# Kernel optimization log

Hardware: AMD Instinct MI355X
Metric: run time of the kernel (lower is better)

## Reference

```python
import jax, jax.numpy as jnp
import numpy as np

N_NODES = 100000
N_EDGES = 1600000
IN_C, HID_C, OUT_C = 128, 128, 64
N_LAYERS, K, ALPHA = 4, 10, 0.1
LN_EPS = 1e-5


def setup_inputs() -> dict:
    key = jax.random.key(0)
    k1, k2, k3, k4, k5 = jax.random.split(key, 5)
    x = jax.random.normal(k1, (N_NODES, IN_C), dtype=jnp.float32)
    edge_index = jax.random.randint(k2, (2, N_EDGES), 0, N_NODES, dtype=jnp.int64)
    edge_weight = jax.random.uniform(k3, (N_EDGES,), dtype=jnp.float32)
    # Learned parameters (torch Linear default init scale ~ 1/sqrt(fan_in))
    W_enc = jax.random.normal(k4, (HID_C, IN_C), dtype=jnp.float32) / np.sqrt(IN_C)
    W_dec = jax.random.normal(k5, (OUT_C, HID_C), dtype=jnp.float32) / np.sqrt(HID_C)
    gamma = jnp.ones((HID_C,), dtype=jnp.float32)
    beta = jnp.zeros((HID_C,), dtype=jnp.float32)
    return {"x": x, "edge_index": edge_index, "edge_weight": edge_weight,
            "W_enc": W_enc, "W_dec": W_dec, "gamma": gamma, "beta": beta}


def _layer_norm(z, gamma, beta):
    mu = jnp.mean(z, axis=-1, keepdims=True)
    var = jnp.mean(jnp.square(z - mu), axis=-1, keepdims=True)
    return gamma * (z - mu) * jax.lax.rsqrt(var + LN_EPS) + beta


def _appnp(h, src, dst, w):
    # K-step personalized-pagerank propagation; normalize=False -> raw edge_weight
    x0 = h
    def step(_, z):
        msg = z[src] * w[:, None]                       # [E, HID_C] gather + scale
        agg = jax.ops.segment_sum(msg, dst, num_segments=N_NODES)  # scatter-add
        return (1.0 - ALPHA) * agg + ALPHA * x0
    return jax.lax.fori_loop(0, K, step, h)


def reference(x, edge_index, edge_weight, W_enc, W_dec, gamma, beta):
    src, dst = edge_index[0], edge_index[1]  # message flows source -> target
    h = x @ W_enc.T
    h = jax.nn.gelu(_layer_norm(h, gamma, beta), approximate=False)
    for _ in range(N_LAYERS):
        h = jax.nn.gelu(_appnp(h, src, dst, edge_weight), approximate=False)
        h = _layer_norm(h, gamma, beta)
    out = h @ W_dec.T
    return jnp.squeeze(out)
```

## Files before the change

### kernel.cpp

```cpp
#include <hip/hip_runtime.h>
#include <math.h>

#define N_NODES 100000
#define N_EDGES 1600000
#define IN_C 128
#define HID_C 128
#define OUT_C 64
#define NLAYERS 4
#define KSTEPS 10
#define ALPHA 0.1f
#define LN_EPS 1e-5f

#define SCAN_N (N_NODES + 1)
#define SCAN_BLOCKS ((SCAN_N + 1023) / 1024)
#define EP_CAP 2400000

__device__ __forceinline__ float gelu_exact(float x) {
    return 0.5f * x * (1.0f + erff(x * 0.70710678118654752f));
}

__device__ __forceinline__ unsigned pack_bf16_rne(float a, float b) {
    unsigned ua = __float_as_uint(a);
    unsigned ub = __float_as_uint(b);
    ua = (ua + 0x7fffu + ((ua >> 16) & 1u)) >> 16;
    ub = (ub + 0x7fffu + ((ub >> 16) & 1u)) >> 16;
    return (ub << 16) | ua;
}
__device__ __forceinline__ float bf_lo(unsigned d) { return __uint_as_float(d << 16); }
__device__ __forceinline__ float bf_hi(unsigned d) { return __uint_as_float(d & 0xffff0000u); }

__global__ void count_k(const int* __restrict__ dst, int* __restrict__ counts) {
    int e = blockIdx.x * blockDim.x + threadIdx.x;
    if (e < N_EDGES) atomicAdd(&counts[dst[e]], 1);
}

__global__ __launch_bounds__(1024) void scan1_k(const int* __restrict__ counts,
                                                int* __restrict__ bsum) {
    __shared__ int s[1024];
    int i = blockIdx.x * 1024 + threadIdx.x;
    int c = 0;
    if (i < N_NODES) c = (counts[i] + 7) & ~7;
    s[threadIdx.x] = c;
    __syncthreads();
    for (int off = 512; off; off >>= 1) {
        if (threadIdx.x < off) s[threadIdx.x] += s[threadIdx.x + off];
        __syncthreads();
    }
    if (threadIdx.x == 0) bsum[blockIdx.x] = s[0];
}

__global__ void scan2_k(int* __restrict__ bsum) {
    __shared__ int s[128];
    int t = threadIdx.x;
    s[t] = (t < SCAN_BLOCKS) ? bsum[t] : 0;
    __syncthreads();
    for (int off = 1; off < 128; off <<= 1) {
        int v = (t >= off) ? s[t - off] : 0;
        __syncthreads();
        s[t] += v;
        __syncthreads();
    }
    if (t < SCAN_BLOCKS) bsum[t] = (t == 0) ? 0 : s[t - 1];
}

__global__ __launch_bounds__(1024) void scan3_k(const int* __restrict__ counts,
                                                const int* __restrict__ bsum,
                                                int* __restrict__ row_off,
                                                int* __restrict__ fill_pos) {
    __shared__ int s[1024];
    int i = blockIdx.x * 1024 + threadIdx.x;
    int c = 0;
    if (i < N_NODES) c = (counts[i] + 7) & ~7;
    s[threadIdx.x] = c;
    __syncthreads();
    for (int off = 1; off < 1024; off <<= 1) {
        int v = (threadIdx.x >= off) ? s[threadIdx.x - off] : 0;
        __syncthreads();
        s[threadIdx.x] += v;
        __syncthreads();
    }
    if (i <= N_NODES) {
        int excl = s[threadIdx.x] - c + bsum[blockIdx.x];
        row_off[i] = excl;
        fill_pos[i] = excl;
    }
}

__global__ void bucket_k(const int* __restrict__ src, const int* __restrict__ dst,
                         const float* __restrict__ w,
                         int* __restrict__ fill_pos, int2* __restrict__ ep) {
    int e = blockIdx.x * blockDim.x + threadIdx.x;
    if (e >= N_EDGES) return;
    int d = dst[e];
    int pos = atomicAdd(&fill_pos[d], 1);
    float ws = (1.0f - ALPHA) * w[e];
    ep[pos] = make_int2(src[e] << 6, __float_as_int(ws));
}

__global__ __launch_bounds__(1024) void encoder_k(
        const float* __restrict__ x, const float* __restrict__ Wenc,
        const float* __restrict__ gamma, const float* __restrict__ beta,
        unsigned* __restrict__ H) {
    __shared__ float WT[IN_C * 130];
    __shared__ float XS[16][512];
    for (int i = threadIdx.x; i < IN_C * HID_C; i += 1024) {
        int c = i >> 7, k = i & 127;
        WT[k * 130 + c] = Wenc[i];
    }
    __syncthreads();
    int lane = threadIdx.x & 63;
    int wid  = threadIdx.x >> 6;
    const float2* WT2 = (const float2*)WT;
    float2 gb = ((const float2*)gamma)[lane];
    float2 bb = ((const float2*)beta)[lane];
    int wstride = gridDim.x * 16;
    float* xs = XS[wid];
    for (int grp = blockIdx.x * 16 + wid; grp * 4 < N_NODES; grp += wstride) {
        int r0 = grp * 4;
        const float4* xr = (const float4*)(x + (size_t)r0 * IN_C);
        ((float4*)xs)[lane]      = xr[lane];
        ((float4*)xs)[64 + lane] = xr[64 + lane];
        __builtin_amdgcn_wave_barrier();
        float a0x = 0, a0y = 0, a1x = 0, a1y = 0;
        float a2x = 0, a2y = 0, a3x = 0, a3y = 0;
        const float4* xs4 = (const float4*)xs;
#pragma unroll 4
        for (int k4 = 0; k4 < 32; ++k4) {
            float4 xv0 = xs4[k4];
            float4 xv1 = xs4[32 + k4];
            float4 xv2 = xs4[64 + k4];
            float4 xv3 = xs4[96 + k4];
            int k = k4 * 4;
            float2 w0 = WT2[(k + 0) * 65 + lane];
            float2 w1 = WT2[(k + 1) * 65 + lane];
            float2 w2 = WT2[(k + 2) * 65 + lane];
            float2 w3 = WT2[(k + 3) * 65 + lane];
#define ENC_ROW(ax, ay, xv)                                      \
            ax = fmaf(xv.x, w0.x, ax); ay = fmaf(xv.x, w0.y, ay); \
            ax = fmaf(xv.y, w1.x, ax); ay = fmaf(xv.y, w1.y, ay); \
            ax = fmaf(xv.z, w2.x, ax); ay = fmaf(xv.z, w2.y, ay); \
            ax = fmaf(xv.w, w3.x, ax); ay = fmaf(xv.w, w3.y, ay);
            ENC_ROW(a0x, a0y, xv0)
            ENC_ROW(a1x, a1y, xv1)
            ENC_ROW(a2x, a2y, xv2)
            ENC_ROW(a3x, a3y, xv3)
#undef ENC_ROW
        }
        __builtin_amdgcn_wave_barrier();
#define ENC_EPI(ax, ay, row)                                               \
        {                                                                   \
            float sum = ax + ay;                                            \
            for (int off = 32; off; off >>= 1) sum += __shfl_xor(sum, off); \
            float mu = sum * (1.0f / 128.0f);                               \
            float d0 = ax - mu, d1 = ay - mu;                               \
            float vs = d0 * d0 + d1 * d1;                                   \
            for (int off = 32; off; off >>= 1) vs += __shfl_xor(vs, off);   \
            float inv = rsqrtf(vs * (1.0f / 128.0f) + LN_EPS);              \
            float o0 = gelu_exact(gb.x * d0 * inv + bb.x);                  \
            float o1 = gelu_exact(gb.y * d1 * inv + bb.y);                  \
            H[(size_t)(row)*64 + lane] = pack_bf16_rne(o0, o1);             \
        }
        ENC_EPI(a0x, a0y, r0)
        ENC_EPI(a1x, a1y, r0 + 1)
        ENC_EPI(a2x, a2y, r0 + 2)
        ENC_EPI(a3x, a3y, r0 + 3)
#undef ENC_EPI
    }
}

__global__ __launch_bounds__(256) void prop_k(
        const unsigned* __restrict__ zin, const unsigned* __restrict__ x0,
        const int* __restrict__ row_off, const int2* __restrict__ ep,
        unsigned* __restrict__ zout, int fuse_ln,
        const float* __restrict__ gamma, const float* __restrict__ beta) {
    int gw = (blockIdx.x * 256 + threadIdx.x) >> 6;
    if (gw >= N_NODES) return;
    int lane = threadIdx.x & 63;
    int s0 = row_off[gw];
    int s1 = row_off[gw + 1];
    float sx = 0.f, sy = 0.f;
    for (int base = s0; base < s1; base += 64) {
        int cnt = min(64, s1 - base);
        int2 p = make_int2(0, 0);
        if (lane < cnt) p = ep[base + lane];
        for (int j = 0; j < cnt; j += 8) {
            int   o0 = __shfl(p.x, j + 0); float w0 = __int_as_float(__shfl(p.y, j + 0));
            int   o1 = __shfl(p.x, j + 1); float w1 = __int_as_float(__shfl(p.y, j + 1));
            int   o2 = __shfl(p.x, j + 2); float w2 = __int_as_float(__shfl(p.y, j + 2));
            int   o3 = __shfl(p.x, j + 3); float w3 = __int_as_float(__shfl(p.y, j + 3));
            int   o4 = __shfl(p.x, j + 4); float w4 = __int_as_float(__shfl(p.y, j + 4));
            int   o5 = __shfl(p.x, j + 5); float w5 = __int_as_float(__shfl(p.y, j + 5));
            int   o6 = __shfl(p.x, j + 6); float w6 = __int_as_float(__shfl(p.y, j + 6));
            int   o7 = __shfl(p.x, j + 7); float w7 = __int_as_float(__shfl(p.y, j + 7));
            unsigned d0 = zin[o0 + lane];
            unsigned d1 = zin[o1 + lane];
            unsigned d2 = zin[o2 + lane];
            unsigned d3 = zin[o3 + lane];
            unsigned d4 = zin[o4 + lane];
            unsigned d5 = zin[o5 + lane];
            unsigned d6 = zin[o6 + lane];
            unsigned d7 = zin[o7 + lane];
            sx = fmaf(w0, bf_lo(d0), sx); sy = fmaf(w0, bf_hi(d0), sy);
            sx = fmaf(w1, bf_lo(d1), sx); sy = fmaf(w1, bf_hi(d1), sy);
            sx = fmaf(w2, bf_lo(d2), sx); sy = fmaf(w2, bf_hi(d2), sy);
            sx = fmaf(w3, bf_lo(d3), sx); sy = fmaf(w3, bf_hi(d3), sy);
            sx = fmaf(w4, bf_lo(d4), sx); sy = fmaf(w4, bf_hi(d4), sy);
            sx = fmaf(w5, bf_lo(d5), sx); sy = fmaf(w5, bf_hi(d5), sy);
            sx = fmaf(w6, bf_lo(d6), sx); sy = fmaf(w6, bf_hi(d6), sy);
            sx = fmaf(w7, bf_lo(d7), sx); sy = fmaf(w7, bf_hi(d7), sy);
        }
    }
    unsigned xd = x0[(size_t)gw * 64 + lane];
    float zx = fmaf(ALPHA, bf_lo(xd), sx);
    float zy = fmaf(ALPHA, bf_hi(xd), sy);
    unsigned od;
    if (fuse_ln) {
        float h0 = gelu_exact(zx);
        float h1 = gelu_exact(zy);
        float sum = h0 + h1;
        for (int off = 32; off; off >>= 1) sum += __shfl_xor(sum, off);
        float mu = sum * (1.0f / 128.0f);
        float d0 = h0 - mu, d1 = h1 - mu;
        float vs = d0 * d0 + d1 * d1;
        for (int off = 32; off; off >>= 1) vs += __shfl_xor(vs, off);
        float inv = rsqrtf(vs * (1.0f / 128.0f) + LN_EPS);
        float2 gb = ((const float2*)gamma)[lane];
        float2 bb = ((const float2*)beta)[lane];
        od = pack_bf16_rne(gb.x * d0 * inv + bb.x, gb.y * d1 * inv + bb.y);
    } else {
        od = pack_bf16_rne(zx, zy);
    }
    zout[(size_t)gw * 64 + lane] = od;
}

__global__ __launch_bounds__(1024) void decoder_k(
        const unsigned* __restrict__ H, const float* __restrict__ Wdec,
        float* __restrict__ out) {
    __shared__ float WT[HID_C * 65];
    __shared__ unsigned XS[16][256];
    for (int i = threadIdx.x; i < OUT_C * HID_C; i += 1024) {
        int o = i >> 7, k = i & 127;
        WT[k * 65 + o] = Wdec[i];
    }
    __syncthreads();
    int lane = threadIdx.x & 63;
    int wid  = threadIdx.x >> 6;
    int wstride = gridDim.x * 16;
    unsigned* xs = XS[wid];
    for (int grp = blockIdx.x * 16 + wid; grp * 4 < N_NODES; grp += wstride) {
        int r0 = grp * 4;
        const unsigned* hp = H + (size_t)r0 * 64;
        xs[lane]       = hp[lane];
        xs[64 + lane]  = hp[64 + lane];
        xs[128 + lane] = hp[128 + lane];
        xs[192 + lane] = hp[192 + lane];
        __builtin_amdgcn_wave_barrier();
        float a0 = 0, a1 = 0, a2 = 0, a3 = 0;
#pragma unroll 4
        for (int k2 = 0; k2 < 64; ++k2) {
            float w0 = WT[(2 * k2) * 65 + lane];
            float w1 = WT[(2 * k2 + 1) * 65 + lane];
            unsigned u0 = xs[k2];
            unsigned u1 = xs[64 + k2];
            unsigned u2 = xs[128 + k2];
            unsigned u3 = xs[192 + k2];
            a0 = fmaf(bf_lo(u0), w0, a0); a0 = fmaf(bf_hi(u0), w1, a0);
            a1 = fmaf(bf_lo(u1), w0, a1); a1 = fmaf(bf_hi(u1), w1, a1);
            a2 = fmaf(bf_lo(u2), w0, a2); a2 = fmaf(bf_hi(u2), w1, a2);
            a3 = fmaf(bf_lo(u3), w0, a3); a3 = fmaf(bf_hi(u3), w1, a3);
        }
        __builtin_amdgcn_wave_barrier();
        out[(size_t)r0 * OUT_C + lane]       = a0;
        out[(size_t)(r0 + 1) * OUT_C + lane] = a1;
        out[(size_t)(r0 + 2) * OUT_C + lane] = a2;
        out[(size_t)(r0 + 3) * OUT_C + lane] = a3;
    }
}

extern "C" void kernel_launch(void* const* d_in, const int* in_sizes, int n_in,
                              void* d_out, int out_size, void* d_ws, size_t ws_size,
                              hipStream_t stream) {
    const float* x     = (const float*)d_in[0];
    const int*   ei    = (const int*)d_in[1];
    const float* ew    = (const float*)d_in[2];
    const float* Wenc  = (const float*)d_in[3];
    const float* Wdec  = (const float*)d_in[4];
    const float* gamma = (const float*)d_in[5];
    const float* beta  = (const float*)d_in[6];
    float* out = (float*)d_out;

    const int* src = ei;
    const int* dst = ei + N_EDGES;

    char* p = (char*)d_ws;
    auto carve = [&](size_t bytes) -> void* {
        void* r = (void*)p;
        p += (bytes + 255) & ~(size_t)255;
        return r;
    };
    int*  counts  = (int*)carve(SCAN_N * sizeof(int));
    int*  fillpos = (int*)carve(SCAN_N * sizeof(int));
    int*  row_off = (int*)carve(SCAN_N * sizeof(int));
    int*  bsum    = (int*)carve(SCAN_BLOCKS * sizeof(int));
    int2* ep      = (int2*)carve((size_t)EP_CAP * sizeof(int2));
    unsigned* H  = (unsigned*)carve((size_t)N_NODES * 64 * sizeof(unsigned));
    unsigned* ZA = (unsigned*)carve((size_t)N_NODES * 64 * sizeof(unsigned));
    unsigned* ZB = (unsigned*)carve((size_t)N_NODES * 64 * sizeof(unsigned));

    hipMemsetAsync(counts, 0, SCAN_N * sizeof(int), stream);
    hipMemsetAsync(ep, 0, (size_t)EP_CAP * sizeof(int2), stream);
    count_k<<<(N_EDGES + 255) / 256, 256, 0, stream>>>(dst, counts);
    scan1_k<<<SCAN_BLOCKS, 1024, 0, stream>>>(counts, bsum);
    scan2_k<<<1, 128, 0, stream>>>(bsum);
    scan3_k<<<SCAN_BLOCKS, 1024, 0, stream>>>(counts, bsum, row_off, fillpos);
    bucket_k<<<(N_EDGES + 255) / 256, 256, 0, stream>>>(src, dst, ew, fillpos, ep);

    encoder_k<<<512, 1024, 0, stream>>>(x, Wenc, gamma, beta, H);

    const int prop_blocks = (N_NODES + 3) / 4;
    unsigned* bufs[2] = {ZA, ZB};
    for (int l = 0; l < NLAYERS; ++l) {
        const unsigned* zin = H;
        for (int k = 0; k < KSTEPS; ++k) {
            int last = (k == KSTEPS - 1);
            unsigned* zout = last ? H : bufs[k & 1];
            prop_k<<<prop_blocks, 256, 0, stream>>>(zin, H, row_off, ep, zout,
                                                    last, gamma, beta);
            zin = zout;
        }
    }

    decoder_k<<<512, 1024, 0, stream>>>(H, Wdec, out);
}
```

Measured before the change: 2.815 ms.

## Chunk edges by source range and assign multiple destination nodes per warp

```diff
diff --git a/kernel.cpp b/kernel.cpp
--- a/kernel.cpp
+++ b/kernel.cpp
@@ -11,14 +11,18 @@
 #define ALPHA 0.1f
 #define LN_EPS 1e-5f
 
-#define SCAN_N (N_NODES + 1)
-#define SCAN_BLOCKS ((SCAN_N + 1023) / 1024)
-#define EP_CAP 2400000
+#define NCHUNK 16
+#define CHUNK_DIV 6250
+#define M2 (NCHUNK * N_NODES)
+#define S2_N (M2 + 1)
+#define S2_BLOCKS ((S2_N + 1023) / 1024)
+
+#define NPW 25
+#define PROP_BLOCKS 1000
 
 __device__ __forceinline__ float gelu_exact(float x) {
     return 0.5f * x * (1.0f + erff(x * 0.70710678118654752f));
 }
-
 __device__ __forceinline__ unsigned pack_bf16_rne(float a, float b) {
     unsigned ua = __float_as_uint(a);
     unsigned ub = __float_as_uint(b);
@@ -29,17 +33,19 @@
 __device__ __forceinline__ float bf_lo(unsigned d) { return __uint_as_float(d << 16); }
 __device__ __forceinline__ float bf_hi(unsigned d) { return __uint_as_float(d & 0xffff0000u); }
 
-__global__ void count_k(const int* __restrict__ dst, int* __restrict__ counts) {
+__global__ void count2_k(const int* __restrict__ src, const int* __restrict__ dst,
+                         int* __restrict__ cnt2) {
     int e = blockIdx.x * blockDim.x + threadIdx.x;
-    if (e < N_EDGES) atomicAdd(&counts[dst[e]], 1);
-}
-
-__global__ __launch_bounds__(1024) void scan1_k(const int* __restrict__ counts,
+    if (e >= N_EDGES) return;
+    int c = src[e] / CHUNK_DIV;
+    atomicAdd(&cnt2[c * N_NODES + dst[e]], 1);
+}
+
+__global__ __launch_bounds__(1024) void scan1_k(const int* __restrict__ cnt2,
                                                 int* __restrict__ bsum) {
     __shared__ int s[1024];
     int i = blockIdx.x * 1024 + threadIdx.x;
-    int c = 0;
-    if (i < N_NODES) c = (counts[i] + 7) & ~7;
+    int c = (i < M2) ? cnt2[i] : 0;
     s[threadIdx.x] = c;
     __syncthreads();
     for (int off = 512; off; off >>= 1) {
@@ -49,28 +55,32 @@
     if (threadIdx.x == 0) bsum[blockIdx.x] = s[0];
 }
 
-__global__ void scan2_k(int* __restrict__ bsum) {
-    __shared__ int s[128];
+__global__ __launch_bounds__(1024) void scan2_k(int* __restrict__ bsum) {
+    __shared__ int s[1024];
     int t = threadIdx.x;
-    s[t] = (t < SCAN_BLOCKS) ? bsum[t] : 0;
-    __syncthreads();
-    for (int off = 1; off < 128; off <<= 1) {
+    int a = (2 * t     < S2_BLOCKS) ? bsum[2 * t]     : 0;
+    int b = (2 * t + 1 < S2_BLOCKS) ? bsum[2 * t + 1] : 0;
+    int tot = a + b;
+    s[t] = tot;
+    __syncthreads();
+    for (int off = 1; off < 1024; off <<= 1) {
         int v = (t >= off) ? s[t - off] : 0;
         __syncthreads();
         s[t] += v;
         __syncthreads();
     }
-    if (t < SCAN_BLOCKS) bsum[t] = (t == 0) ? 0 : s[t - 1];
-}
-
-__global__ __launch_bounds__(1024) void scan3_k(const int* __restrict__ counts,
+    int excl = s[t] - tot;
+    if (2 * t     < S2_BLOCKS) bsum[2 * t]     = excl;
+    if (2 * t + 1 < S2_BLOCKS) bsum[2 * t + 1] = excl + a;
+}
+
+__global__ __launch_bounds__(1024) void scan3_k(const int* __restrict__ cnt2,
                                                 const int* __restrict__ bsum,
-                                                int* __restrict__ row_off,
-                                                int* __restrict__ fill_pos) {
+                                                int* __restrict__ off2,
+                                                int* __restrict__ fill2) {
     __shared__ int s[1024];
     int i = blockIdx.x * 1024 + threadIdx.x;
-    int c = 0;
-    if (i < N_NODES) c = (counts[i] + 7) & ~7;
+    int c = (i < M2) ? cnt2[i] : 0;
     s[threadIdx.x] = c;
     __syncthreads();
     for (int off = 1; off < 1024; off <<= 1) {
@@ -79,22 +89,22 @@
         s[threadIdx.x] += v;
         __syncthreads();
     }
-    if (i <= N_NODES) {
+    if (i <= M2) {
         int excl = s[threadIdx.x] - c + bsum[blockIdx.x];
-        row_off[i] = excl;
-        fill_pos[i] = excl;
-    }
-}
-
-__global__ void bucket_k(const int* __restrict__ src, const int* __restrict__ dst,
-                         const float* __restrict__ w,
-                         int* __restrict__ fill_pos, int2* __restrict__ ep) {
+        off2[i] = excl;
+        fill2[i] = excl;
+    }
+}
+
+__global__ void bucket2_k(const int* __restrict__ src, const int* __restrict__ dst,
+                          const float* __restrict__ w, int* __restrict__ fill2,
+                          int2* __restrict__ ep) {
     int e = blockIdx.x * blockDim.x + threadIdx.x;
     if (e >= N_EDGES) return;
-    int d = dst[e];
-    int pos = atomicAdd(&fill_pos[d], 1);
-    float ws = (1.0f - ALPHA) * w[e];
-    ep[pos] = make_int2(src[e] << 6, __float_as_int(ws));
+    int sv = src[e];
+    int c = sv / CHUNK_DIV;
+    int pos = atomicAdd(&fill2[c * N_NODES + dst[e]], 1);
+    ep[pos] = make_int2(sv << 6, __float_as_int((1.0f - ALPHA) * w[e]));
 }
 
 __global__ __launch_bounds__(1024) void encoder_k(
@@ -168,69 +178,75 @@
     }
 }
 
-__global__ __launch_bounds__(256) void prop_k(
+__global__ __launch_bounds__(256, 4) void prop_k(
         const unsigned* __restrict__ zin, const unsigned* __restrict__ x0,
-        const int* __restrict__ row_off, const int2* __restrict__ ep,
+        const int* __restrict__ off2, const int2* __restrict__ ep,
         unsigned* __restrict__ zout, int fuse_ln,
         const float* __restrict__ gamma, const float* __restrict__ beta) {
-    int gw = (blockIdx.x * 256 + threadIdx.x) >> 6;
-    if (gw >= N_NODES) return;
+    int W = (blockIdx.x * 256 + threadIdx.x) >> 6;
     int lane = threadIdx.x & 63;
-    int s0 = row_off[gw];
-    int s1 = row_off[gw + 1];
-    float sx = 0.f, sy = 0.f;
-    for (int base = s0; base < s1; base += 64) {
-        int cnt = min(64, s1 - base);
+    int nbase = W * NPW;
+    float ax[NPW], ay[NPW];
+#pragma unroll
+    for (int i = 0; i < NPW; ++i) { ax[i] = 0.f; ay[i] = 0.f; }
+#pragma unroll 1
+    for (int c = 0; c < NCHUNK; ++c) {
+        int bidx = c * N_NODES + nbase;
+        int bv = off2[bidx + min(lane, NPW)];
+        int E1 = __shfl(bv, NPW);
+        int wbase = __shfl(bv, 0);
+        int cursor = wbase;
+        int cnt = min(64, E1 - wbase);
         int2 p = make_int2(0, 0);
-        if (lane < cnt) p = ep[base + lane];
-        for (int j = 0; j < cnt; j += 8) {
-            int   o0 = __shfl(p.x, j + 0); float w0 = __int_as_float(__shfl(p.y, j + 0));
-            int   o1 = __shfl(p.x, j + 1); float w1 = __int_as_float(__shfl(p.y, j + 1));
-            int   o2 = __shfl(p.x, j + 2); float w2 = __int_as_float(__shfl(p.y, j + 2));
-            int   o3 = __shfl(p.x, j + 3); float w3 = __int_as_float(__shfl(p.y, j + 3));
-            int   o4 = __shfl(p.x, j + 4); float w4 = __int_as_float(__shfl(p.y, j + 4));
-            int   o5 = __shfl(p.x, j + 5); float w5 = __int_as_float(__shfl(p.y, j + 5));
-            int   o6 = __shfl(p.x, j + 6); float w6 = __int_as_float(__shfl(p.y, j + 6));
-            int   o7 = __shfl(p.x, j + 7); float w7 = __int_as_float(__shfl(p.y, j + 7));
-            unsigned d0 = zin[o0 + lane];
-            unsigned d1 = zin[o1 + lane];
-            unsigned d2 = zin[o2 + lane];
-            unsigned d3 = zin[o3 + lane];
-            unsigned d4 = zin[o4 + lane];
-            unsigned d5 = zin[o5 + lane];
-            unsigned d6 = zin[o6 + lane];
-            unsigned d7 = zin[o7 + lane];
-            sx = fmaf(w0, bf_lo(d0), sx); sy = fmaf(w0, bf_hi(d0), sy);
-            sx = fmaf(w1, bf_lo(d1), sx); sy = fmaf(w1, bf_hi(d1), sy);
-            sx = fmaf(w2, bf_lo(d2), sx); sy = fmaf(w2, bf_hi(d2), sy);
-            sx = fmaf(w3, bf_lo(d3), sx); sy = fmaf(w3, bf_hi(d3), sy);
-            sx = fmaf(w4, bf_lo(d4), sx); sy = fmaf(w4, bf_hi(d4), sy);
-            sx = fmaf(w5, bf_lo(d5), sx); sy = fmaf(w5, bf_hi(d5), sy);
-            sx = fmaf(w6, bf_lo(d6), sx); sy = fmaf(w6, bf_hi(d6), sy);
-            sx = fmaf(w7, bf_lo(d7), sx); sy = fmaf(w7, bf_hi(d7), sy);
-        }
-    }
-    unsigned xd = x0[(size_t)gw * 64 + lane];
-    float zx = fmaf(ALPHA, bf_lo(xd), sx);
-    float zy = fmaf(ALPHA, bf_hi(xd), sy);
-    unsigned od;
+        if (lane < cnt) p = ep[wbase + lane];
+#pragma unroll
+        for (int i = 0; i < NPW; ++i) {
+            int eend = __shfl(bv, i + 1);
+            while (cursor < eend) {
+                int j = cursor - wbase;
+                if (j >= cnt) {
+                    wbase = cursor;
+                    cnt = min(64, E1 - wbase);
+                    p = make_int2(0, 0);
+                    if (lane < cnt) p = ep[wbase + lane];
+                    j = 0;
+                }
+                int px = __shfl(p.x, j);
+                float w = __int_as_float(__shfl(p.y, j));
+                unsigned v = zin[px + lane];
+                ax[i] = fmaf(w, bf_lo(v), ax[i]);
+                ay[i] = fmaf(w, bf_hi(v), ay[i]);
+                ++cursor;
+            }
+        }
+    }
+    float2 gb = make_float2(0.f, 0.f), bb = make_float2(0.f, 0.f);
     if (fuse_ln) {
-        float h0 = gelu_exact(zx);
-        float h1 = gelu_exact(zy);
-        float sum = h0 + h1;
-        for (int off = 32; off; off >>= 1) sum += __shfl_xor(sum, off);
-        float mu = sum * (1.0f / 128.0f);
-        float d0 = h0 - mu, d1 = h1 - mu;
-        float vs = d0 * d0 + d1 * d1;
-        for (int off = 32; off; off >>= 1) vs += __shfl_xor(vs, off);
-        float inv = rsqrtf(vs * (1.0f / 128.0f) + LN_EPS);
-        float2 gb = ((const float2*)gamma)[lane];
-        float2 bb = ((const float2*)beta)[lane];
-        od = pack_bf16_rne(gb.x * d0 * inv + bb.x, gb.y * d1 * inv + bb.y);
-    } else {
-        od = pack_bf16_rne(zx, zy);
-    }
-    zout[(size_t)gw * 64 + lane] = od;
+        gb = ((const float2*)gamma)[lane];
+        bb = ((const float2*)beta)[lane];
+    }
+#pragma unroll
+    for (int i = 0; i < NPW; ++i) {
+        int n = nbase + i;
+        unsigned xd = x0[(size_t)n * 64 + lane];
+        float zx = fmaf(ALPHA, bf_lo(xd), ax[i]);
+        float zy = fmaf(ALPHA, bf_hi(xd), ay[i]);
+        unsigned od;
+        if (fuse_ln) {
+            float h0 = gelu_exact(zx), h1 = gelu_exact(zy);
+            float sum = h0 + h1;
+            for (int off = 32; off; off >>= 1) sum += __shfl_xor(sum, off);
+            float mu = sum * (1.0f / 128.0f);
+            float d0 = h0 - mu, d1 = h1 - mu;
+            float vs = d0 * d0 + d1 * d1;
+            for (int off = 32; off; off >>= 1) vs += __shfl_xor(vs, off);
+            float inv = rsqrtf(vs * (1.0f / 128.0f) + LN_EPS);
+            od = pack_bf16_rne(gb.x * d0 * inv + bb.x, gb.y * d1 * inv + bb.y);
+        } else {
+            od = pack_bf16_rne(zx, zy);
+        }
+        zout[(size_t)n * 64 + lane] = od;
+    }
 }
 
 __global__ __launch_bounds__(1024) void decoder_k(
@@ -298,33 +314,31 @@
         p += (bytes + 255) & ~(size_t)255;
         return r;
     };
-    int*  counts  = (int*)carve(SCAN_N * sizeof(int));
-    int*  fillpos = (int*)carve(SCAN_N * sizeof(int));
-    int*  row_off = (int*)carve(SCAN_N * sizeof(int));
-    int*  bsum    = (int*)carve(SCAN_BLOCKS * sizeof(int));
-    int2* ep      = (int2*)carve((size_t)EP_CAP * sizeof(int2));
+    int*  cnt2  = (int*)carve((size_t)M2 * sizeof(int));
+    int*  fill2 = (int*)carve((size_t)(M2 + 1) * sizeof(int));
+    int*  off2  = (int*)carve((size_t)(M2 + 1) * sizeof(int));
+    int*  bsum  = (int*)carve(S2_BLOCKS * sizeof(int));
+    int2* ep    = (int2*)carve((size_t)N_EDGES * sizeof(int2));
     unsigned* H  = (unsigned*)carve((size_t)N_NODES * 64 * sizeof(unsigned));
     unsigned* ZA = (unsigned*)carve((size_t)N_NODES * 64 * sizeof(unsigned));
     unsigned* ZB = (unsigned*)carve((size_t)N_NODES * 64 * sizeof(unsigned));
 
-    hipMemsetAsync(counts, 0, SCAN_N * sizeof(int), stream);
-    hipMemsetAsync(ep, 0, (size_t)EP_CAP * sizeof(int2), stream);
-    count_k<<<(N_EDGES + 255) / 256, 256, 0, stream>>>(dst, counts);
-    scan1_k<<<SCAN_BLOCKS, 1024, 0, stream>>>(counts, bsum);
-    scan2_k<<<1, 128, 0, stream>>>(bsum);
-    scan3_k<<<SCAN_BLOCKS, 1024, 0, stream>>>(counts, bsum, row_off, fillpos);
-    bucket_k<<<(N_EDGES + 255) / 256, 256, 0, stream>>>(src, dst, ew, fillpos, ep);
+    hipMemsetAsync(cnt2, 0, (size_t)M2 * sizeof(int), stream);
+    count2_k<<<(N_EDGES + 255) / 256, 256, 0, stream>>>(src, dst, cnt2);
+    scan1_k<<<S2_BLOCKS, 1024, 0, stream>>>(cnt2, bsum);
+    scan2_k<<<1, 1024, 0, stream>>>(bsum);
+    scan3_k<<<S2_BLOCKS, 1024, 0, stream>>>(cnt2, bsum, off2, fill2);
+    bucket2_k<<<(N_EDGES + 255) / 256, 256, 0, stream>>>(src, dst, ew, fill2, ep);
 
     encoder_k<<<512, 1024, 0, stream>>>(x, Wenc, gamma, beta, H);
 
-    const int prop_blocks = (N_NODES + 3) / 4;
     unsigned* bufs[2] = {ZA, ZB};
     for (int l = 0; l < NLAYERS; ++l) {
         const unsigned* zin = H;
         for (int k = 0; k < KSTEPS; ++k) {
             int last = (k == KSTEPS - 1);
             unsigned* zout = last ? H : bufs[k & 1];
-            prop_k<<<prop_blocks, 256, 0, stream>>>(zin, H, row_off, ep, zout,
+            prop_k<<<PROP_BLOCKS, 256, 0, stream>>>(zin, H, off2, ep, zout,
                                                     last, gamma, beta);
             zin = zout;
         }
```

Result: slower. 8.167 ms (+190.1%).

## Fuse all propagation steps into one persistent cooperative kernel with grid sync

Applied to the files above, without the earlier changes.

```diff
diff --git a/kernel.cpp b/kernel.cpp
--- a/kernel.cpp
+++ b/kernel.cpp
@@ -1,5 +1,8 @@
 #include <hip/hip_runtime.h>
+#include <hip/hip_cooperative_groups.h>
 #include <math.h>
+
+namespace cg = cooperative_groups;
 
 #define N_NODES 100000
 #define N_EDGES 1600000
@@ -14,11 +17,11 @@
 #define SCAN_N (N_NODES + 1)
 #define SCAN_BLOCKS ((SCAN_N + 1023) / 1024)
 #define EP_CAP 2400000
+#define PROP_GRID 1024
 
 __device__ __forceinline__ float gelu_exact(float x) {
     return 0.5f * x * (1.0f + erff(x * 0.70710678118654752f));
 }
-
 __device__ __forceinline__ unsigned pack_bf16_rne(float a, float b) {
     unsigned ua = __float_as_uint(a);
     unsigned ub = __float_as_uint(b);
@@ -168,69 +171,82 @@
     }
 }
 
-__global__ __launch_bounds__(256) void prop_k(
-        const unsigned* __restrict__ zin, const unsigned* __restrict__ x0,
+__global__ __launch_bounds__(256, 4) void prop_all_k(
         const int* __restrict__ row_off, const int2* __restrict__ ep,
-        unsigned* __restrict__ zout, int fuse_ln,
+        unsigned* __restrict__ H, unsigned* __restrict__ ZA,
+        unsigned* __restrict__ ZB,
         const float* __restrict__ gamma, const float* __restrict__ beta) {
-    int gw = (blockIdx.x * 256 + threadIdx.x) >> 6;
-    if (gw >= N_NODES) return;
+    cg::grid_group grid = cg::this_grid();
     int lane = threadIdx.x & 63;
-    int s0 = row_off[gw];
-    int s1 = row_off[gw + 1];
-    float sx = 0.f, sy = 0.f;
-    for (int base = s0; base < s1; base += 64) {
-        int cnt = min(64, s1 - base);
-        int2 p = make_int2(0, 0);
-        if (lane < cnt) p = ep[base + lane];
-        for (int j = 0; j < cnt; j += 8) {
-            int   o0 = __shfl(p.x, j + 0); float w0 = __int_as_float(__shfl(p.y, j + 0));
-            int   o1 = __shfl(p.x, j + 1); float w1 = __int_as_float(__shfl(p.y, j + 1));
-            int   o2 = __shfl(p.x, j + 2); float w2 = __int_as_float(__shfl(p.y, j + 2));
-            int   o3 = __shfl(p.x, j + 3); float w3 = __int_as_float(__shfl(p.y, j + 3));
-            int   o4 = __shfl(p.x, j + 4); float w4 = __int_as_float(__shfl(p.y, j + 4));
-            int   o5 = __shfl(p.x, j + 5); float w5 = __int_as_float(__shfl(p.y, j + 5));
-            int   o6 = __shfl(p.x, j + 6); float w6 = __int_as_float(__shfl(p.y, j + 6));
-            int   o7 = __shfl(p.x, j + 7); float w7 = __int_as_float(__shfl(p.y, j + 7));
-            unsigned d0 = zin[o0 + lane];
-            unsigned d1 = zin[o1 + lane];
-            unsigned d2 = zin[o2 + lane];
-            unsigned d3 = zin[o3 + lane];
-            unsigned d4 = zin[o4 + lane];
-            unsigned d5 = zin[o5 + lane];
-            unsigned d6 = zin[o6 + lane];
-            unsigned d7 = zin[o7 + lane];
-            sx = fmaf(w0, bf_lo(d0), sx); sy = fmaf(w0, bf_hi(d0), sy);
-            sx = fmaf(w1, bf_lo(d1), sx); sy = fmaf(w1, bf_hi(d1), sy);
-            sx = fmaf(w2, bf_lo(d2), sx); sy = fmaf(w2, bf_hi(d2), sy);
-            sx = fmaf(w3, bf_lo(d3), sx); sy = fmaf(w3, bf_hi(d3), sy);
-            sx = fmaf(w4, bf_lo(d4), sx); sy = fmaf(w4, bf_hi(d4), sy);
-            sx = fmaf(w5, bf_lo(d5), sx); sy = fmaf(w5, bf_hi(d5), sy);
-            sx = fmaf(w6, bf_lo(d6), sx); sy = fmaf(w6, bf_hi(d6), sy);
-            sx = fmaf(w7, bf_lo(d7), sx); sy = fmaf(w7, bf_hi(d7), sy);
+    int wave0 = (blockIdx.x * 256 + threadIdx.x) >> 6;
+    const int NW = (PROP_GRID * 256) >> 6;
+    float2 gb = ((const float2*)gamma)[lane];
+    float2 bb = ((const float2*)beta)[lane];
+    unsigned* bufs[2] = {ZA, ZB};
+    for (int l = 0; l < NLAYERS; ++l) {
+        const unsigned* zin = H;
+        for (int k = 0; k < KSTEPS; ++k) {
+            int last = (k == KSTEPS - 1);
+            unsigned* zout = last ? H : bufs[k & 1];
+            for (int gw = wave0; gw < N_NODES; gw += NW) {
+                int s0 = row_off[gw];
+                int s1 = row_off[gw + 1];
+                float sx = 0.f, sy = 0.f;
+                for (int base = s0; base < s1; base += 64) {
+                    int cnt = min(64, s1 - base);
+                    int2 p = make_int2(0, 0);
+                    if (lane < cnt) p = ep[base + lane];
+                    for (int j = 0; j < cnt; j += 8) {
+                        int   o0 = __shfl(p.x, j + 0); float w0 = __int_as_float(__shfl(p.y, j + 0));
+                        int   o1 = __shfl(p.x, j + 1); float w1 = __int_as_float(__shfl(p.y, j + 1));
+                        int   o2 = __shfl(p.x, j + 2); float w2 = __int_as_float(__shfl(p.y, j + 2));
+                        int   o3 = __shfl(p.x, j + 3); float w3 = __int_as_float(__shfl(p.y, j + 3));
+                        int   o4 = __shfl(p.x, j + 4); float w4 = __int_as_float(__shfl(p.y, j + 4));
+                        int   o5 = __shfl(p.x, j + 5); float w5 = __int_as_float(__shfl(p.y, j + 5));
+                        int   o6 = __shfl(p.x, j + 6); float w6 = __int_as_float(__shfl(p.y, j + 6));
+                        int   o7 = __shfl(p.x, j + 7); float w7 = __int_as_float(__shfl(p.y, j + 7));
+                        unsigned d0 = zin[o0 + lane];
+                        unsigned d1 = zin[o1 + lane];
+                        unsigned d2 = zin[o2 + lane];
+                        unsigned d3 = zin[o3 + lane];
+                        unsigned d4 = zin[o4 + lane];
+                        unsigned d5 = zin[o5 + lane];
+                        unsigned d6 = zin[o6 + lane];
+                        unsigned d7 = zin[o7 + lane];
+                        sx = fmaf(w0, bf_lo(d0), sx); sy = fmaf(w0, bf_hi(d0), sy);
+                        sx = fmaf(w1, bf_lo(d1), sx); sy = fmaf(w1, bf_hi(d1), sy);
+                        sx = fmaf(w2, bf_lo(d2), sx); sy = fmaf(w2, bf_hi(d2), sy);
+                        sx = fmaf(w3, bf_lo(d3), sx); sy = fmaf(w3, bf_hi(d3), sy);
+                        sx = fmaf(w4, bf_lo(d4), sx); sy = fmaf(w4, bf_hi(d4), sy);
+                        sx = fmaf(w5, bf_lo(d5), sx); sy = fmaf(w5, bf_hi(d5), sy);
+                        sx = fmaf(w6, bf_lo(d6), sx); sy = fmaf(w6, bf_hi(d6), sy);
+                        sx = fmaf(w7, bf_lo(d7), sx); sy = fmaf(w7, bf_hi(d7), sy);
+                    }
+                }
+                unsigned xd = H[(size_t)gw * 64 + lane];
+                float zx = fmaf(ALPHA, bf_lo(xd), sx);
+                float zy = fmaf(ALPHA, bf_hi(xd), sy);
+                unsigned od;
+                if (last) {
+                    float h0 = gelu_exact(zx);
+                    float h1 = gelu_exact(zy);
+                    float sum = h0 + h1;
+                    for (int off = 32; off; off >>= 1) sum += __shfl_xor(sum, off);
+                    float mu = sum * (1.0f / 128.0f);
+                    float d0 = h0 - mu, d1 = h1 - mu;
+                    float vs = d0 * d0 + d1 * d1;
+                    for (int off = 32; off; off >>= 1) vs += __shfl_xor(vs, off);
+                    float inv = rsqrtf(vs * (1.0f / 128.0f) + LN_EPS);
+                    od = pack_bf16_rne(gb.x * d0 * inv + bb.x, gb.y * d1 * inv + bb.y);
+                } else {
+                    od = pack_bf16_rne(zx, zy);
+                }
+                zout[(size_t)gw * 64 + lane] = od;
+            }
+            grid.sync();
+            zin = zout;
         }
     }
-    unsigned xd = x0[(size_t)gw * 64 + lane];
-    float zx = fmaf(ALPHA, bf_lo(xd), sx);
-    float zy = fmaf(ALPHA, bf_hi(xd), sy);
-    unsigned od;
-    if (fuse_ln) {
-        float h0 = gelu_exact(zx);
-        float h1 = gelu_exact(zy);
-        float sum = h0 + h1;
-        for (int off = 32; off; off >>= 1) sum += __shfl_xor(sum, off);
-        float mu = sum * (1.0f / 128.0f);
-        float d0 = h0 - mu, d1 = h1 - mu;
-        float vs = d0 * d0 + d1 * d1;
-        for (int off = 32; off; off >>= 1) vs += __shfl_xor(vs, off);
-        float inv = rsqrtf(vs * (1.0f / 128.0f) + LN_EPS);
-        float2 gb = ((const float2*)gamma)[lane];
-        float2 bb = ((const float2*)beta)[lane];
-        od = pack_bf16_rne(gb.x * d0 * inv + bb.x, gb.y * d1 * inv + bb.y);
-    } else {
-        od = pack_bf16_rne(zx, zy);
-    }
-    zout[(size_t)gw * 64 + lane] = od;
 }
 
 __global__ __launch_bounds__(1024) void decoder_k(
@@ -317,17 +333,14 @@
 
     encoder_k<<<512, 1024, 0, stream>>>(x, Wenc, gamma, beta, H);
 
-    const int prop_blocks = (N_NODES + 3) / 4;
-    unsigned* bufs[2] = {ZA, ZB};
-    for (int l = 0; l < NLAYERS; ++l) {
-        const unsigned* zin = H;
-        for (int k = 0; k < KSTEPS; ++k) {
-            int last = (k == KSTEPS - 1);
-            unsigned* zout = last ? H : bufs[k & 1];
-            prop_k<<<prop_blocks, 256, 0, stream>>>(zin, H, row_off, ep, zout,
-                                                    last, gamma, beta);
-            zin = zout;
-        }
+    {
+        const int* ro = row_off; const int2* epp = ep;
+        unsigned *h = H, *za = ZA, *zb = ZB;
+        const float *g = gamma, *b = beta;
+        void* args[] = {(void*)&ro, (void*)&epp, (void*)&h, (void*)&za,
+                        (void*)&zb, (void*)&g, (void*)&b};
+        hipLaunchCooperativeKernel((void*)prop_all_k, dim3(PROP_GRID), dim3(256),
+                                   args, 0, stream);
     }
 
     decoder_k<<<512, 1024, 0, stream>>>(H, Wdec, out);
```

Measured after the change: 8.297 ms. +194.7%, slower.
